# Kernel optimization log

Measured on AMD Instinct MI355X. Metric: run time of the kernel, lower is better.

## Reference

```python
import jax, jax.numpy as jnp
import numpy as np

D = 512      # dim_model
F = 2048     # dim_feedforward
E = 8        # num_experts
K = 2        # num_experts_per_token
B, S = 2, 4096


def setup_inputs() -> dict:
    key = jax.random.key(0)
    ks = jax.random.split(key, 8)
    sd = 1.0 / np.sqrt(D)
    sf = 1.0 / np.sqrt(F)
    return {
        "x": jax.random.normal(ks[0], (B, S, D), dtype=jnp.float32),
        "router_w": jax.random.uniform(ks[1], (D, E), jnp.float32, -sd, sd),
        "router_b": jax.random.uniform(ks[2], (E,), jnp.float32, -sd, sd),
        "w1": jax.random.uniform(ks[3], (E, D, F), jnp.float32, -sd, sd),
        "b1": jax.random.uniform(ks[4], (E, F), jnp.float32, -sd, sd),
        "w2": jax.random.uniform(ks[5], (E, F, D), jnp.float32, -sf, sf),
        "b2": jax.random.uniform(ks[6], (E, D), jnp.float32, -sf, sf),
    }


def reference(x, router_w, router_b, w1, b1, w2, b2):
    orig_shape = x.shape
    flat = x.reshape(-1, orig_shape[-1])                     # [T, D]
    logits = flat @ router_w + router_b                      # [T, E]
    gates = jax.nn.softmax(logits, axis=-1)                  # [T, E]
    top_vals, top_idx = jax.lax.top_k(gates, K)              # [T, K]
    top_vals = top_vals / jnp.sum(top_vals, axis=-1, keepdims=True)
    # combine weight per (token, expert): zero for unselected experts,
    # so dense per-expert evaluation yields identical math to masked dispatch.
    onehot = jax.nn.one_hot(top_idx, E, dtype=flat.dtype)    # [T, K, E]
    comb = jnp.einsum('tk,tke->te', top_vals, onehot)        # [T, E]
    # expert FFNs over all tokens (dropout is identity in eval)
    hidden = jax.nn.relu(jnp.einsum('td,edf->etf', flat, w1) + b1[:, None, :])  # [E, T, F]
    eout = jnp.einsum('etf,efd->etd', hidden, w2) + b2[:, None, :]              # [E, T, D]
    out = jnp.einsum('te,etd->td', comb, eout)               # [T, D]
    return out.reshape(orig_shape)
```

## Files before the change

### kernel.cpp

```cpp
#include <hip/hip_runtime.h>
#include <cstdint>
#include <cstddef>

#define TD 512
#define TF 2048
#define NE 8
#define NT 8192
#define CAP 17408

using u16 = unsigned short;
using u32 = unsigned int;

typedef __attribute__((ext_vector_type(8))) __bf16 bf16x8;
typedef __attribute__((ext_vector_type(4))) float f32x4;

__device__ __forceinline__ u16 f2bf(float f) {
  u32 u = __float_as_uint(f);
  u32 r = (u + 0x7fffu + ((u >> 16) & 1u)) >> 16;
  return (u16)r;
}

__device__ __forceinline__ float bf2f(u16 b) {
  return __uint_as_float((u32)b << 16);
}

__device__ __forceinline__ void load_lds16(const void* g, void* l) {
  __builtin_amdgcn_global_load_lds(
      (const __attribute__((address_space(1))) void*)g,
      (__attribute__((address_space(3))) void*)l, 16, 0, 0);
}

__device__ __forceinline__ void transpose64(const float* __restrict__ ib,
                                            u16* __restrict__ ob, int R, int C,
                                            int r0, int c0, u16* tile ) {
  const int tid = threadIdx.x;
  const int l16 = tid & 15;
  const int grp = tid >> 4;
  #pragma unroll
  for (int p = 0; p < 4; p++) {
    int r = p * 16 + grp;
    float4 v = *reinterpret_cast<const float4*>(ib + (size_t)(r0 + r) * C + c0 + l16 * 4);
    u16 o[4] = {f2bf(v.x), f2bf(v.y), f2bf(v.z), f2bf(v.w)};
    *reinterpret_cast<uint2*>(&tile[r * 68 + l16 * 4]) = *reinterpret_cast<uint2*>(o);
  }
  __syncthreads();
  #pragma unroll
  for (int p = 0; p < 4; p++) {
    int c = p * 16 + grp;
    int rr = l16 * 4;
    u16 o[4] = {tile[(rr + 0) * 68 + c], tile[(rr + 1) * 68 + c],
                tile[(rr + 2) * 68 + c], tile[(rr + 3) * 68 + c]};
    *reinterpret_cast<uint2*>(ob + (size_t)(c0 + c) * R + r0 + rr) = *reinterpret_cast<uint2*>(o);
  }
}

__global__ void prep_kernel(const float* __restrict__ x, const float* __restrict__ rw,
                            const float* __restrict__ rb, int2* __restrict__ tokE,
                            float2* __restrict__ tokG, u16* __restrict__ xb,
                            const float* __restrict__ w1, u16* __restrict__ w1t,
                            const float* __restrict__ w2, u16* __restrict__ w2t,
                            int* __restrict__ ghist) {
  __shared__ u16 tile[64 * 68];
  int b = blockIdx.x;
  if (b < NT / 4) {
    if (b == 0 && threadIdx.x < 16) ghist[threadIdx.x] = 0;
    int wv = threadIdx.x >> 6;
    int lane = threadIdx.x & 63;
    int t = b * 4 + wv;
    const float* xr = x + (size_t)t * TD;
    float4 a0 = *reinterpret_cast<const float4*>(xr + lane * 4);
    float4 a1 = *reinterpret_cast<const float4*>(xr + 256 + lane * 4);
    {
      u16 o[8];
      o[0] = f2bf(a0.x); o[1] = f2bf(a0.y); o[2] = f2bf(a0.z); o[3] = f2bf(a0.w);
      o[4] = f2bf(a1.x); o[5] = f2bf(a1.y); o[6] = f2bf(a1.z); o[7] = f2bf(a1.w);
      u16* xo = xb + (size_t)t * TD;
      *reinterpret_cast<uint2*>(xo + lane * 4) = *reinterpret_cast<uint2*>(o);
      *reinterpret_cast<uint2*>(xo + 256 + lane * 4) = *reinterpret_cast<uint2*>(o + 4);
    }
    float p[NE];
    #pragma unroll
    for (int e = 0; e < NE; e++) p[e] = 0.f;
    float av[8] = {a0.x, a0.y, a0.z, a0.w, a1.x, a1.y, a1.z, a1.w};
    #pragma unroll
    for (int j = 0; j < 8; j++) {
      int d = (j < 4) ? (lane * 4 + j) : (256 + lane * 4 + j - 4);
      const float* r = rw + (size_t)d * NE;
      #pragma unroll
      for (int e = 0; e < NE; e++) p[e] += av[j] * r[e];
    }
    #pragma unroll
    for (int off = 32; off >= 1; off >>= 1) {
      #pragma unroll
      for (int e = 0; e < NE; e++) p[e] += __shfl_xor(p[e], off);
    }
    if (lane == 0) {
      float l[NE];
      #pragma unroll
      for (int e = 0; e < NE; e++) l[e] = p[e] + rb[e];
      float m = l[0];
      #pragma unroll
      for (int e = 1; e < NE; e++) m = fmaxf(m, l[e]);
      float g[NE];
      #pragma unroll
      for (int e = 0; e < NE; e++) g[e] = __expf(l[e] - m);
      int i0 = 0;
      #pragma unroll
      for (int e = 1; e < NE; e++) if (g[e] > g[i0]) i0 = e;
      int i1 = -1;
      #pragma unroll
      for (int e = 0; e < NE; e++) {
        if (e == i0) continue;
        if (i1 < 0 || g[e] > g[i1]) i1 = e;
      }
      float inv = 1.f / (g[i0] + g[i1]);
      tokE[t] = make_int2(i0, i1);
      tokG[t] = make_float2(g[i0] * inv, g[i1] * inv);
    }
  } else {
    int tb = b - NT / 4;
    int which = tb >> 11;
    int idx = tb & 2047;
    int e = idx >> 8;
    int tl = idx & 255;
    if (which == 0) {
      int rt = tl >> 5, ct = tl & 31;
      transpose64(w1 + (size_t)e * TD * TF, w1t + (size_t)e * TD * TF,
                  TD, TF, rt * 64, ct * 64, tile);
    } else {
      int rt = tl >> 3, ct = tl & 7;
      transpose64(w2 + (size_t)e * TF * TD, w2t + (size_t)e * TF * TD,
                  TF, TD, rt * 64, ct * 64, tile);
    }
  }
}

__global__ void hist_kernel(const int2* __restrict__ tokE, int* __restrict__ ghist,
                            int* __restrict__ offs, int* __restrict__ cnt,
                            int* __restrict__ cursors) {
  __shared__ int h[NE];
  __shared__ int last;
  if (threadIdx.x < NE) h[threadIdx.x] = 0;
  __syncthreads();
  int t = blockIdx.x * 256 + threadIdx.x;
  int2 e = tokE[t];
  atomicAdd(&h[e.x], 1);
  atomicAdd(&h[e.y], 1);
  __syncthreads();
  if (threadIdx.x < NE) atomicAdd(&ghist[threadIdx.x], h[threadIdx.x]);
  __threadfence();
  if (threadIdx.x == 0) last = (atomicAdd(&ghist[15], 1) == 31);
  __syncthreads();
  if (last) {
    if (threadIdx.x == 0) {
      int tot = 0;
      for (int i = 0; i < NE; i++) {
        int hv = atomicAdd(&ghist[i], 0);
        offs[i] = tot;
        cnt[i] = hv;
        tot += (hv + 127) & ~127;
      }
      offs[NE] = tot;
    }
    if (threadIdx.x < NE) cursors[threadIdx.x * 16] = 0;
  }
}

__global__ void scatter_kernel(const int2* __restrict__ tokE,
                               const int* __restrict__ offs, int* __restrict__ cursors,
                               int* __restrict__ tok, int* __restrict__ slotOf) {
  int t = blockIdx.x * 256 + threadIdx.x;
  int lane = threadIdx.x & 63;
  int2 e = tokE[t];
  #pragma unroll
  for (int k = 0; k < 2; k++) {
    int ek = k ? e.y : e.x;
    #pragma unroll
    for (int ex = 0; ex < NE; ex++) {
      unsigned long long mask = __ballot(ek == ex);
      if (ek == ex) {
        int leader = __ffsll(mask) - 1;
        int rank = __popcll(mask & ((1ull << lane) - 1ull));
        int base = 0;
        if (lane == leader) base = atomicAdd(&cursors[ex * 16], __popcll(mask));
        base = __shfl(base, leader);
        int s = offs[ex] + base + rank;
        tok[s] = t;
        slotOf[t * 2 + k] = s;
      }
    }
  }
}

__global__ __launch_bounds__(256, 3) void gemm1_kernel(
    const u16* __restrict__ xb, const u16* __restrict__ w1t,
    const float* __restrict__ b1, const int* __restrict__ tok,
    const int* __restrict__ offs, const int* __restrict__ cnt,
    u16* __restrict__ H) {
  __shared__ u16 As[128 * 64];
  __shared__ u16 Bs[128 * 64];
  __shared__ int tokS[128];
  const int tid = threadIdx.x;
  const int s0 = blockIdx.x * 128;
  const int f0 = blockIdx.y * 128;
  int e = 0;
  #pragma unroll
  for (int i = 1; i <= 7; i++)
    if (s0 >= offs[i]) e = i;
  const int vend = offs[e] + cnt[e];
  if (tid < 128) {
    int s = s0 + tid;
    tokS[tid] = (s < vend) ? tok[s] : 0;
  }
  __syncthreads();

  const int lane = tid & 63;
  const int wv = tid >> 6;
  const int srow = lane >> 3;
  const int scol = (((lane & 7) ^ srow) & 7) * 8;
  const int wm = (wv >> 1) * 64;
  const int wn = (wv & 1) * 64;
  const int mrow = lane & 15;
  const int quad = lane >> 4;
  const int rq = mrow & 7;

  f32x4 zero = {0.f, 0.f, 0.f, 0.f};
  f32x4 acc[4][4];
  #pragma unroll
  for (int i = 0; i < 4; i++)
    #pragma unroll
    for (int j = 0; j < 4; j++) acc[i][j] = zero;

  const u16* bbase = w1t + ((size_t)e * TF + f0) * TD;

  for (int k0 = 0; k0 < TD; k0 += 64) {
    if (k0) __syncthreads();
    #pragma unroll
    for (int p = 0; p < 4; p++) {
      int row = wv * 32 + p * 8 + srow;
      load_lds16(xb + (size_t)tokS[row] * TD + k0 + scol, &As[(wv * 32 + p * 8) * 64]);
      load_lds16(bbase + (size_t)row * TD + k0 + scol, &Bs[(wv * 32 + p * 8) * 64]);
    }
    __syncthreads();
    #pragma unroll
    for (int ks = 0; ks < 2; ks++) {
      bf16x8 a[4], b[4];
      #pragma unroll
      for (int i = 0; i < 4; i++)
        a[i] = *reinterpret_cast<const bf16x8*>(
            &As[(wm + i * 16 + mrow) * 64 + ((ks * 4 + quad) ^ rq) * 8]);
      #pragma unroll
      for (int j = 0; j < 4; j++)
        b[j] = *reinterpret_cast<const bf16x8*>(
            &Bs[(wn + j * 16 + mrow) * 64 + ((ks * 4 + quad) ^ rq) * 8]);
      #pragma unroll
      for (int i = 0; i < 4; i++)
        #pragma unroll
        for (int j = 0; j < 4; j++)
          acc[i][j] = __builtin_amdgcn_mfma_f32_16x16x32_bf16(a[i], b[j], acc[i][j], 0, 0, 0);
    }
  }

  float bv[4];
  #pragma unroll
  for (int j = 0; j < 4; j++) bv[j] = b1[e * TF + f0 + wn + j * 16 + mrow];
  #pragma unroll
  for (int i = 0; i < 4; i++) {
    #pragma unroll
    for (int r = 0; r < 4; r++) {
      int row = s0 + wm + i * 16 + quad * 4 + r;
      u16* hrow = H + (size_t)row * TF + f0;
      #pragma unroll
      for (int j = 0; j < 4; j++) {
        float v = acc[i][j][r] + bv[j];
        v = v > 0.f ? v : 0.f;
        hrow[wn + j * 16 + mrow] = f2bf(v);
      }
    }
  }
}

__global__ __launch_bounds__(256, 3) void gemm2_kernel(
    const u16* __restrict__ H, const u16* __restrict__ w2t,
    const float* __restrict__ b2, const int* __restrict__ offs,
    u16* __restrict__ eout) {
  __shared__ u16 As[128 * 64];
  __shared__ u16 Bs[128 * 64];
  const int tid = threadIdx.x;
  const int s0 = blockIdx.x * 128;
  const int d0 = blockIdx.y * 128;
  int e = 0;
  #pragma unroll
  for (int i = 1; i <= 7; i++)
    if (s0 >= offs[i]) e = i;

  const int lane = tid & 63;
  const int wv = tid >> 6;
  const int srow = lane >> 3;
  const int scol = (((lane & 7) ^ srow) & 7) * 8;
  const int wm = (wv >> 1) * 64;
  const int wn = (wv & 1) * 64;
  const int mrow = lane & 15;
  const int quad = lane >> 4;
  const int rq = mrow & 7;

  f32x4 zero = {0.f, 0.f, 0.f, 0.f};
  f32x4 acc[4][4];
  #pragma unroll
  for (int i = 0; i < 4; i++)
    #pragma unroll
    for (int j = 0; j < 4; j++) acc[i][j] = zero;

  const u16* bbase = w2t + ((size_t)e * TD + d0) * TF;

  for (int k0 = 0; k0 < TF; k0 += 64) {
    if (k0) __syncthreads();
    #pragma unroll
    for (int p = 0; p < 4; p++) {
      int row = wv * 32 + p * 8 + srow;
      load_lds16(H + (size_t)(s0 + row) * TF + k0 + scol, &As[(wv * 32 + p * 8) * 64]);
      load_lds16(bbase + (size_t)row * TF + k0 + scol, &Bs[(wv * 32 + p * 8) * 64]);
    }
    __syncthreads();
    #pragma unroll
    for (int ks = 0; ks < 2; ks++) {
      bf16x8 a[4], b[4];
      #pragma unroll
      for (int i = 0; i < 4; i++)
        a[i] = *reinterpret_cast<const bf16x8*>(
            &As[(wm + i * 16 + mrow) * 64 + ((ks * 4 + quad) ^ rq) * 8]);
      #pragma unroll
      for (int j = 0; j < 4; j++)
        b[j] = *reinterpret_cast<const bf16x8*>(
            &Bs[(wn + j * 16 + mrow) * 64 + ((ks * 4 + quad) ^ rq) * 8]);
      #pragma unroll
      for (int i = 0; i < 4; i++)
        #pragma unroll
        for (int j = 0; j < 4; j++)
          acc[i][j] = __builtin_amdgcn_mfma_f32_16x16x32_bf16(a[i], b[j], acc[i][j], 0, 0, 0);
    }
  }

  float bv[4];
  #pragma unroll
  for (int j = 0; j < 4; j++) bv[j] = b2[e * TD + d0 + wn + j * 16 + mrow];
  #pragma unroll
  for (int i = 0; i < 4; i++) {
    #pragma unroll
    for (int r = 0; r < 4; r++) {
      int row = s0 + wm + i * 16 + quad * 4 + r;
      u16* orow = eout + (size_t)row * TD + d0;
      #pragma unroll
      for (int j = 0; j < 4; j++) {
        orow[wn + j * 16 + mrow] = f2bf(acc[i][j][r] + bv[j]);
      }
    }
  }
}

__global__ void combine_kernel(const u16* __restrict__ eout, const int* __restrict__ slotOf,
                               const float2* __restrict__ tokG, float* __restrict__ out) {
  int wv = threadIdx.x >> 6;
  int lane = threadIdx.x & 63;
  int t = blockIdx.x * 4 + wv;
  int sA = slotOf[t * 2];
  int sB = slotOf[t * 2 + 1];
  float2 g = tokG[t];
  uint4 ua = *reinterpret_cast<const uint4*>(eout + (size_t)sA * TD + lane * 8);
  uint4 ub = *reinterpret_cast<const uint4*>(eout + (size_t)sB * TD + lane * 8);
  const u16* pa = reinterpret_cast<const u16*>(&ua);
  const u16* pb = reinterpret_cast<const u16*>(&ub);
  float o[8];
  #pragma unroll
  for (int k = 0; k < 8; k++) o[k] = g.x * bf2f(pa[k]) + g.y * bf2f(pb[k]);
  float* od = out + (size_t)t * TD + lane * 8;
  *reinterpret_cast<float4*>(od) = make_float4(o[0], o[1], o[2], o[3]);
  *reinterpret_cast<float4*>(od + 4) = make_float4(o[4], o[5], o[6], o[7]);
}

extern "C" void kernel_launch(void* const* d_in, const int* in_sizes, int n_in,
                              void* d_out, int out_size, void* d_ws, size_t ws_size,
                              hipStream_t stream) {
  const float* x  = (const float*)d_in[0];
  const float* rw = (const float*)d_in[1];
  const float* rb = (const float*)d_in[2];
  const float* w1 = (const float*)d_in[3];
  const float* b1 = (const float*)d_in[4];
  const float* w2 = (const float*)d_in[5];
  const float* b2 = (const float*)d_in[6];
  float* out = (float*)d_out;

  char* w = (char*)d_ws;
  u16* xb    = (u16*)w;           w += (size_t)NT * TD * 2;
  u16* w1t   = (u16*)w;           w += (size_t)NE * TD * TF * 2;
  u16* w2t   = (u16*)w;           w += (size_t)NE * TF * TD * 2;
  u16* H     = (u16*)w;           w += (size_t)CAP * TF * 2;
  u16* eout  = (u16*)w;           w += (size_t)CAP * TD * 2;
  int* tok   = (int*)w;           w += (size_t)CAP * 4;
  int* slotOf = (int*)w;          w += (size_t)NT * 2 * 4;
  int2* tokE = (int2*)w;          w += (size_t)NT * 8;
  float2* tokG = (float2*)w;      w += (size_t)NT * 8;
  int* ghist = (int*)w;           w += 256;
  int* cursors = (int*)w;         w += 1024;
  int* offs  = (int*)w;           w += 256;
  int* cnt   = (int*)w;           w += 256;

  prep_kernel<<<dim3(NT / 4 + 4096), dim3(256), 0, stream>>>(
      x, rw, rb, tokE, tokG, xb, w1, w1t, w2, w2t, ghist);
  hist_kernel<<<dim3(32), dim3(256), 0, stream>>>(tokE, ghist, offs, cnt, cursors);
  scatter_kernel<<<dim3(NT / 256), dim3(256), 0, stream>>>(tokE, offs, cursors, tok, slotOf);
  gemm1_kernel<<<dim3(CAP / 128, TF / 128), dim3(256), 0, stream>>>(xb, w1t, b1, tok, offs, cnt, H);
  gemm2_kernel<<<dim3(CAP / 128, TD / 128), dim3(256), 0, stream>>>(H, w2t, b2, offs, eout);
  combine_kernel<<<dim3(NT / 4), dim3(256), 0, stream>>>(eout, slotOf, tokG, out);
}
```

Before: 267.2 us.

## Load expert weight fragments directly into registers with prefetch, dropping LDS B tile

Both expert GEMMs now read their weight (B) operand straight from global memory into registers, laid out in MFMA fragment order, and prefetch the next k-step while the current one computes. This removes the B shared-memory tile and its LDS reads. Each weight row is now read separately by both wave pairs that use it, so global and L2 traffic per block rises. The extra live registers led to lowering launch bounds from 3 to 2 waves per SIMD, and gemm1's hidden activations are written with nontemporal stores.

Measured after the change: 357.6 us. 33.8% more time.

```diff
diff --git a/kernel.cpp b/kernel.cpp
--- a/kernel.cpp
+++ b/kernel.cpp
@@ -192,13 +192,12 @@
   }
 }
 
-__global__ __launch_bounds__(256, 3) void gemm1_kernel(
+__global__ __launch_bounds__(256, 2) void gemm1_kernel(
     const u16* __restrict__ xb, const u16* __restrict__ w1t,
     const float* __restrict__ b1, const int* __restrict__ tok,
     const int* __restrict__ offs, const int* __restrict__ cnt,
     u16* __restrict__ H) {
   __shared__ u16 As[128 * 64];
-  __shared__ u16 Bs[128 * 64];
   __shared__ int tokS[128];
   const int tid = threadIdx.x;
   const int s0 = blockIdx.x * 128;
@@ -223,6 +222,12 @@
   const int mrow = lane & 15;
   const int quad = lane >> 4;
   const int rq = mrow & 7;
+  const int koff = quad * 8;
+
+  const u16* brow[4];
+  #pragma unroll
+  for (int j = 0; j < 4; j++)
+    brow[j] = w1t + ((size_t)e * TF + f0 + wn + j * 16 + mrow) * TD;
 
   f32x4 zero = {0.f, 0.f, 0.f, 0.f};
   f32x4 acc[4][4];
@@ -231,7 +236,12 @@
     #pragma unroll
     for (int j = 0; j < 4; j++) acc[i][j] = zero;
 
-  const u16* bbase = w1t + ((size_t)e * TF + f0) * TD;
+  bf16x8 bc[2][4], bn[2][4];
+  #pragma unroll
+  for (int ks = 0; ks < 2; ks++)
+    #pragma unroll
+    for (int j = 0; j < 4; j++)
+      bc[ks][j] = *reinterpret_cast<const bf16x8*>(brow[j] + ks * 32 + koff);
 
   for (int k0 = 0; k0 < TD; k0 += 64) {
     if (k0) __syncthreads();
@@ -239,26 +249,34 @@
     for (int p = 0; p < 4; p++) {
       int row = wv * 32 + p * 8 + srow;
       load_lds16(xb + (size_t)tokS[row] * TD + k0 + scol, &As[(wv * 32 + p * 8) * 64]);
-      load_lds16(bbase + (size_t)row * TD + k0 + scol, &Bs[(wv * 32 + p * 8) * 64]);
+    }
+    int kn = k0 + 64;
+    if (kn < TD) {
+      #pragma unroll
+      for (int ks = 0; ks < 2; ks++)
+        #pragma unroll
+        for (int j = 0; j < 4; j++)
+          bn[ks][j] = *reinterpret_cast<const bf16x8*>(brow[j] + kn + ks * 32 + koff);
     }
     __syncthreads();
     #pragma unroll
     for (int ks = 0; ks < 2; ks++) {
-      bf16x8 a[4], b[4];
+      bf16x8 a[4];
       #pragma unroll
       for (int i = 0; i < 4; i++)
         a[i] = *reinterpret_cast<const bf16x8*>(
             &As[(wm + i * 16 + mrow) * 64 + ((ks * 4 + quad) ^ rq) * 8]);
       #pragma unroll
-      for (int j = 0; j < 4; j++)
-        b[j] = *reinterpret_cast<const bf16x8*>(
-            &Bs[(wn + j * 16 + mrow) * 64 + ((ks * 4 + quad) ^ rq) * 8]);
-      #pragma unroll
       for (int i = 0; i < 4; i++)
         #pragma unroll
         for (int j = 0; j < 4; j++)
-          acc[i][j] = __builtin_amdgcn_mfma_f32_16x16x32_bf16(a[i], b[j], acc[i][j], 0, 0, 0);
-    }
+          acc[i][j] = __builtin_amdgcn_mfma_f32_16x16x32_bf16(a[i], bc[ks][j], acc[i][j], 0, 0, 0);
+    }
+    #pragma unroll
+    for (int ks = 0; ks < 2; ks++)
+      #pragma unroll
+      for (int j = 0; j < 4; j++)
+        bc[ks][j] = bn[ks][j];
   }
 
   float bv[4];
@@ -274,18 +292,17 @@
       for (int j = 0; j < 4; j++) {
         float v = acc[i][j][r] + bv[j];
         v = v > 0.f ? v : 0.f;
-        hrow[wn + j * 16 + mrow] = f2bf(v);
+        __builtin_nontemporal_store(f2bf(v), &hrow[wn + j * 16 + mrow]);
       }
     }
   }
 }
 
-__global__ __launch_bounds__(256, 3) void gemm2_kernel(
+__global__ __launch_bounds__(256, 2) void gemm2_kernel(
     const u16* __restrict__ H, const u16* __restrict__ w2t,
     const float* __restrict__ b2, const int* __restrict__ offs,
     u16* __restrict__ eout) {
   __shared__ u16 As[128 * 64];
-  __shared__ u16 Bs[128 * 64];
   const int tid = threadIdx.x;
   const int s0 = blockIdx.x * 128;
   const int d0 = blockIdx.y * 128;
@@ -303,6 +320,12 @@
   const int mrow = lane & 15;
   const int quad = lane >> 4;
   const int rq = mrow & 7;
+  const int koff = quad * 8;
+
+  const u16* brow[4];
+  #pragma unroll
+  for (int j = 0; j < 4; j++)
+    brow[j] = w2t + ((size_t)e * TD + d0 + wn + j * 16 + mrow) * TF;
 
   f32x4 zero = {0.f, 0.f, 0.f, 0.f};
   f32x4 acc[4][4];
@@ -311,7 +334,12 @@
     #pragma unroll
     for (int j = 0; j < 4; j++) acc[i][j] = zero;
 
-  const u16* bbase = w2t + ((size_t)e * TD + d0) * TF;
+  bf16x8 bc[2][4], bn[2][4];
+  #pragma unroll
+  for (int ks = 0; ks < 2; ks++)
+    #pragma unroll
+    for (int j = 0; j < 4; j++)
+      bc[ks][j] = *reinterpret_cast<const bf16x8*>(brow[j] + ks * 32 + koff);
 
   for (int k0 = 0; k0 < TF; k0 += 64) {
     if (k0) __syncthreads();
@@ -319,26 +347,34 @@
     for (int p = 0; p < 4; p++) {
       int row = wv * 32 + p * 8 + srow;
       load_lds16(H + (size_t)(s0 + row) * TF + k0 + scol, &As[(wv * 32 + p * 8) * 64]);
-      load_lds16(bbase + (size_t)row * TF + k0 + scol, &Bs[(wv * 32 + p * 8) * 64]);
+    }
+    int kn = k0 + 64;
+    if (kn < TF) {
+      #pragma unroll
+      for (int ks = 0; ks < 2; ks++)
+        #pragma unroll
+        for (int j = 0; j < 4; j++)
+          bn[ks][j] = *reinterpret_cast<const bf16x8*>(brow[j] + kn + ks * 32 + koff);
     }
     __syncthreads();
     #pragma unroll
     for (int ks = 0; ks < 2; ks++) {
-      bf16x8 a[4], b[4];
+      bf16x8 a[4];
       #pragma unroll
       for (int i = 0; i < 4; i++)
         a[i] = *reinterpret_cast<const bf16x8*>(
             &As[(wm + i * 16 + mrow) * 64 + ((ks * 4 + quad) ^ rq) * 8]);
       #pragma unroll
-      for (int j = 0; j < 4; j++)
-        b[j] = *reinterpret_cast<const bf16x8*>(
-            &Bs[(wn + j * 16 + mrow) * 64 + ((ks * 4 + quad) ^ rq) * 8]);
-      #pragma unroll
       for (int i = 0; i < 4; i++)
         #pragma unroll
         for (int j = 0; j < 4; j++)
-          acc[i][j] = __builtin_amdgcn_mfma_f32_16x16x32_bf16(a[i], b[j], acc[i][j], 0, 0, 0);
-    }
+          acc[i][j] = __builtin_amdgcn_mfma_f32_16x16x32_bf16(a[i], bc[ks][j], acc[i][j], 0, 0, 0);
+    }
+    #pragma unroll
+    for (int ks = 0; ks < 2; ks++)
+      #pragma unroll
+      for (int j = 0; j < 4; j++)
+        bc[ks][j] = bn[ks][j];
   }
 
   float bv[4];
```
